# Kernel tuning notes

Hardware: AMD Instinct MI355X
Metric: run time of the kernel (lower is better)

The kernel has to match this reference:

```python
import jax, jax.numpy as jnp
import numpy as np

N = 100_000      # num_nodes
E = 1_600_000    # num_edges (avg degree 16)
D = 64           # embedding_dim
L = 3            # num_layers


def setup_inputs() -> dict:
    key = jax.random.key(0)
    k1, k2 = jax.random.split(key)
    edge_index = jax.random.randint(k1, (2, E), 0, N, dtype=jnp.int64)
    edge_weight = jnp.ones((E,), jnp.float32)
    # nn.init.normal_(std=0.1)
    embedding = 0.1 * jax.random.normal(k2, (N, D), dtype=jnp.float32)
    return {"embedding": embedding, "edge_weight": edge_weight, "edge_index": edge_index}


def reference(embedding, edge_weight, edge_index):
    n = embedding.shape[0]
    self_idx = jnp.arange(n, dtype=edge_index.dtype)
    # add_self_loops: append (i, i) with weight 1 (PyG default fill_value)
    row = jnp.concatenate([edge_index[0], self_idx])  # source j
    col = jnp.concatenate([edge_index[1], self_idx])  # target i
    ew = jnp.concatenate([edge_weight, jnp.ones((n,), embedding.dtype)])
    # degree() counts occurrences of row (unweighted)
    deg = jax.ops.segment_sum(jnp.ones_like(ew), row, num_segments=n)
    deg_inv_sqrt = jnp.where(deg > 0, jax.lax.rsqrt(deg), 0.0)
    norm = deg_inv_sqrt[row] * ew * deg_inv_sqrt[col]  # [E+N]

    x = embedding
    acc = embedding  # running sum of layer-0..L embeddings
    for _ in range(L):
        # gather from source, scale, scatter-add to target (dropout off in eval)
        msg = norm[:, None] * x[row]                       # [E+N, D]
        x = jax.ops.segment_sum(msg, col, num_segments=n)  # [N, D]
        acc = acc + x
    return acc / (L + 1)
```

## Files before the change

### kernel.cpp

```cpp
#include <hip/hip_runtime.h>
#include <stdint.h>

#define DIM 64
#define GB 256
#define GSH 8
#define CH 2048
#define TB1 256
#define HW 25000
#define NSL 256
#define TBH 1024

__device__ __forceinline__ unsigned bf16rne(float f) {
    unsigned u = __float_as_uint(f);
    return (u + 0x7FFFu + ((u >> 16) & 1u)) >> 16;
}
__device__ __forceinline__ unsigned pack2(float lo, float hi) {
    return bf16rne(lo) | (bf16rne(hi) << 16);
}
#define UNPK(u, lo, hi) { lo = __uint_as_float((u) << 16); hi = __uint_as_float((u) & 0xFFFF0000u); }

__global__ void __launch_bounds__(TBH)
hist_kernel(const int* __restrict__ src, const int* __restrict__ dst,
            unsigned* __restrict__ partials, int* __restrict__ bslice,
            int E, int N, int Es, int NB) {
    __shared__ unsigned h8[HW];
    __shared__ int hb[512];
    const int s = blockIdx.x;
    const int nw = (N + 3) >> 2;
    for (int j = threadIdx.x; j < nw; j += TBH) h8[j] = 0;
    for (int j = threadIdx.x; j < 512; j += TBH) hb[j] = 0;
    __syncthreads();
    const int e0 = s * Es, e1 = min(e0 + Es, E);
#pragma unroll 4
    for (int i = e0 + threadIdx.x; i < e1; i += TBH) {
        unsigned sj = (unsigned)src[i];
        unsigned tj = (unsigned)dst[i];
        atomicAdd(&h8[sj >> 2], 1u << ((sj & 3) * 8));
        atomicAdd(&hb[tj >> GSH], 1);
    }
    __syncthreads();
    unsigned* part = partials + (size_t)s * nw;
    for (int j = threadIdx.x; j < nw; j += TBH) part[j] = h8[j];
    for (int j = threadIdx.x; j < NB; j += TBH) bslice[s * 512 + j] = hb[j];
}

__global__ void __launch_bounds__(512)
merge_scan_kernel(const unsigned* __restrict__ partials, const int* __restrict__ bslice,
                  float* __restrict__ dis, int* __restrict__ bucket_base,
                  int* __restrict__ cursor, int* __restrict__ offsets,
                  int nw, int nmerge, int N, int NB) {
    __shared__ int buf[512];
    if ((int)blockIdx.x < nmerge) {
        const int w = blockIdx.x * 512 + threadIdx.x;
        if (w >= nw) return;
        int s0 = 0, s1 = 0, s2 = 0, s3 = 0;
#pragma unroll 8
        for (int s = 0; s < NSL; ++s) {
            unsigned v = partials[(size_t)s * nw + w];
            s0 += v & 255u; s1 += (v >> 8) & 255u;
            s2 += (v >> 16) & 255u; s3 += v >> 24;
        }
        const int nidx = w * 4;
        if (nidx + 3 < N) {
            *(float4*)(dis + nidx) = make_float4(
                rsqrtf((float)s0 + 1.f), rsqrtf((float)s1 + 1.f),
                rsqrtf((float)s2 + 1.f), rsqrtf((float)s3 + 1.f));
        } else {
            if (nidx + 0 < N) dis[nidx + 0] = rsqrtf((float)s0 + 1.f);
            if (nidx + 1 < N) dis[nidx + 1] = rsqrtf((float)s1 + 1.f);
            if (nidx + 2 < N) dis[nidx + 2] = rsqrtf((float)s2 + 1.f);
            if (nidx + 3 < N) dis[nidx + 3] = rsqrtf((float)s3 + 1.f);
        }
    } else {
        const int t = threadIdx.x;
        int v = 0;
        if (t < NB)
            for (int s = 0; s < NSL; ++s) v += bslice[s * 512 + t];
        buf[t] = v;
        __syncthreads();
        for (int off = 1; off < 512; off <<= 1) {
            int add = (t >= off) ? buf[t - off] : 0;
            __syncthreads();
            buf[t] += add;
            __syncthreads();
        }
        if (t < NB) { bucket_base[t] = buf[t] - v; cursor[t] = buf[t] - v; }
        if (t == NB - 1) { bucket_base[NB] = buf[t]; offsets[N] = buf[t]; }
    }
}

__global__ void __launch_bounds__(TB1)
part_conv_kernel(const int* __restrict__ src, const int* __restrict__ dst,
                 const float* __restrict__ ew,
                 int* __restrict__ cursor, int2* __restrict__ staged,
                 const float4* __restrict__ emb4, uint4* __restrict__ x0c,
                 int E, int NB, int npart, int n8) {
    __shared__ int h[512];
    if ((int)blockIdx.x >= npart) {
        const int i = (blockIdx.x - npart) * TB1 + threadIdx.x;
        if (i >= n8) return;
        float4 a = emb4[2 * i], b = emb4[2 * i + 1];
        uint4 o;
        o.x = pack2(a.x, a.y); o.y = pack2(a.z, a.w);
        o.z = pack2(b.x, b.y); o.w = pack2(b.z, b.w);
        x0c[i] = o;
        return;
    }
    const int tid = threadIdx.x;
    const int e0 = blockIdx.x * CH;
    const int e1 = min(e0 + CH, E);
    for (int j = tid; j < 512; j += TB1) h[j] = 0;
    __syncthreads();
    int4 d[CH / (TB1 * 4)];
    int ngrp = 0;
    for (int i = e0 + tid * 4, k = 0; i < e1; i += TB1 * 4, ++k) {
        int4 t;
        if (i + 3 < e1) t = *(const int4*)(dst + i);
        else {
            t.x = dst[i];
            t.y = (i + 1 < e1) ? dst[i + 1] : -1;
            t.z = (i + 2 < e1) ? dst[i + 2] : -1;
            t.w = (i + 3 < e1) ? dst[i + 3] : -1;
        }
        d[k] = t;
        if (t.x >= 0) atomicAdd(&h[t.x >> GSH], 1);
        if (t.y >= 0) atomicAdd(&h[t.y >> GSH], 1);
        if (t.z >= 0) atomicAdd(&h[t.z >> GSH], 1);
        if (t.w >= 0) atomicAdd(&h[t.w >> GSH], 1);
        ngrp = k + 1;
    }
    __syncthreads();
    for (int j = tid; j < NB; j += TB1) {
        int c = h[j];
        h[j] = c ? atomicAdd(&cursor[j], c) : 0;
    }
    __syncthreads();
    for (int i = e0 + tid * 4, k = 0; k < ngrp; i += TB1 * 4, ++k) {
        int4 t = d[k];
        int4 ss = make_int4(0, 0, 0, 0);
        float4 ww = make_float4(0.f, 0.f, 0.f, 0.f);
        if (i + 3 < e1) { ss = *(const int4*)(src + i); ww = *(const float4*)(ew + i); }
        else {
            ss.x = src[i]; ww.x = ew[i];
            if (i + 1 < e1) { ss.y = src[i + 1]; ww.y = ew[i + 1]; }
            if (i + 2 < e1) { ss.z = src[i + 2]; ww.z = ew[i + 2]; }
            if (i + 3 < e1) { ss.w = src[i + 3]; ww.w = ew[i + 3]; }
        }
#define PART1(T, S, W) if ((T) >= 0) { \
        int pos_ = atomicAdd(&h[(T) >> GSH], 1); \
        staged[pos_] = make_int2((S) | (((T) & (GB - 1)) << 20), __float_as_int(W)); }
        PART1(t.x, ss.x, ww.x)
        PART1(t.y, ss.y, ww.y)
        PART1(t.z, ss.z, ww.z)
        PART1(t.w, ss.w, ww.w)
#undef PART1
    }
}

__global__ void __launch_bounds__(256)
place_kernel(const int2* __restrict__ staged, const int* __restrict__ bucket_base,
             const float* __restrict__ dis,
             int* __restrict__ offsets, int2* __restrict__ csr, int N) {
    __shared__ int cnt[GB];
    __shared__ int cur[GB];
    __shared__ int pre[GB + 1];
    __shared__ float disb[GB];
    const int b = blockIdx.x;
    const int n0 = b << GSH;
    const int nb = min(GB, N - n0);
    const int r0 = bucket_base[b], r1 = bucket_base[b + 1];
    cnt[threadIdx.x] = 0;
    disb[threadIdx.x] = (threadIdx.x < nb) ? dis[n0 + threadIdx.x] : 0.f;
    __syncthreads();
    for (int i = r0 + threadIdx.x; i < r1; i += 256)
        atomicAdd(&cnt[(staged[i].x >> 20) & (GB - 1)], 1);
    __syncthreads();
    if (threadIdx.x == 0) {
        int run = r0;
        for (int j = 0; j < nb; ++j) { pre[j] = run; run += cnt[j]; }
        pre[nb] = run;
    }
    __syncthreads();
    if (threadIdx.x < nb) { offsets[n0 + threadIdx.x] = pre[threadIdx.x]; cur[threadIdx.x] = pre[threadIdx.x]; }
    __syncthreads();
    for (int i = r0 + threadIdx.x; i < r1; i += 256) {
        int2 rec = staged[i];
        int tl = (rec.x >> 20) & (GB - 1);
        int s = rec.x & 0xFFFFF;
        int rank = atomicAdd(&cur[tl], 1);
        float w = dis[s] * __int_as_float(rec.y) * disb[tl];
        csr[rank] = make_int2(s, __float_as_int(w));
    }
}

__global__ void __launch_bounds__(256)
prop_kernel(const uint4* __restrict__ xg, const float4* __restrict__ selfF,
            uint4* __restrict__ xstore,
            const int* __restrict__ offsets, const int2* __restrict__ csr,
            const float* __restrict__ dis, int n,
            const float4* __restrict__ embF, const uint4* __restrict__ xaF,
            float4* __restrict__ outF) {
    const int lane = threadIdx.x & 63;
    const int fl  = lane & 7;
    const int sub = lane >> 3;
    const int wave = blockIdx.x * (blockDim.x >> 6) + (threadIdx.x >> 6);
    const int node = wave * 8 + sub;
    if (node >= n) return;

    const int beg = offsets[node];
    const int end = offsets[node + 1];
    const float d = dis[node];
    const float dd = d * d;

    float a0, a1, a2, a3, a4, a5, a6, a7;
    uint4 qs = make_uint4(0, 0, 0, 0);
    if (selfF) {
        float4 s0 = selfF[(size_t)node * 16 + fl * 2];
        float4 s1 = selfF[(size_t)node * 16 + fl * 2 + 1];
        a0 = dd * s0.x; a1 = dd * s0.y; a2 = dd * s0.z; a3 = dd * s0.w;
        a4 = dd * s1.x; a5 = dd * s1.y; a6 = dd * s1.z; a7 = dd * s1.w;
    } else {
        qs = xg[(size_t)node * 8 + fl];
        float l, h;
        UNPK(qs.x, l, h) a0 = dd * l; a1 = dd * h;
        UNPK(qs.y, l, h) a2 = dd * l; a3 = dd * h;
        UNPK(qs.z, l, h) a4 = dd * l; a5 = dd * h;
        UNPK(qs.w, l, h) a6 = dd * l; a7 = dd * h;
    }

#define EDGE(E, Q) { float w_ = __int_as_float((E).y); float l, h; \
    UNPK((Q).x, l, h) a0 = fmaf(w_, l, a0); a1 = fmaf(w_, h, a1); \
    UNPK((Q).y, l, h) a2 = fmaf(w_, l, a2); a3 = fmaf(w_, h, a3); \
    UNPK((Q).z, l, h) a4 = fmaf(w_, l, a4); a5 = fmaf(w_, h, a5); \
    UNPK((Q).w, l, h) a6 = fmaf(w_, l, a6); a7 = fmaf(w_, h, a7); }

    int p = beg;
    for (; p + 8 <= end; p += 8) {
        int2 e0 = csr[p + 0], e1 = csr[p + 1], e2 = csr[p + 2], e3 = csr[p + 3];
        int2 e4 = csr[p + 4], e5 = csr[p + 5], e6 = csr[p + 6], e7 = csr[p + 7];
        uint4 q0 = xg[(size_t)e0.x * 8 + fl];
        uint4 q1 = xg[(size_t)e1.x * 8 + fl];
        uint4 q2 = xg[(size_t)e2.x * 8 + fl];
        uint4 q3 = xg[(size_t)e3.x * 8 + fl];
        uint4 q4 = xg[(size_t)e4.x * 8 + fl];
        uint4 q5 = xg[(size_t)e5.x * 8 + fl];
        uint4 q6 = xg[(size_t)e6.x * 8 + fl];
        uint4 q7 = xg[(size_t)e7.x * 8 + fl];
        EDGE(e0, q0) EDGE(e1, q1) EDGE(e2, q2) EDGE(e3, q3)
        EDGE(e4, q4) EDGE(e5, q5) EDGE(e6, q6) EDGE(e7, q7)
    }
    for (; p + 4 <= end; p += 4) {
        int2 e0 = csr[p + 0], e1 = csr[p + 1], e2 = csr[p + 2], e3 = csr[p + 3];
        uint4 q0 = xg[(size_t)e0.x * 8 + fl];
        uint4 q1 = xg[(size_t)e1.x * 8 + fl];
        uint4 q2 = xg[(size_t)e2.x * 8 + fl];
        uint4 q3 = xg[(size_t)e3.x * 8 + fl];
        EDGE(e0, q0) EDGE(e1, q1) EDGE(e2, q2) EDGE(e3, q3)
    }
    for (; p < end; ++p) {
        int2 e = csr[p];
        uint4 q = xg[(size_t)e.x * 8 + fl];
        EDGE(e, q)
    }
#undef EDGE

    if (outF) {
        float4 eA = embF[(size_t)node * 16 + fl * 2];
        float4 eB = embF[(size_t)node * 16 + fl * 2 + 1];
        uint4 qa = xaF[(size_t)node * 8 + fl];
        float r0 = eA.x + a0, r1 = eA.y + a1, r2 = eA.z + a2, r3 = eA.w + a3;
        float r4 = eB.x + a4, r5 = eB.y + a5, r6 = eB.z + a6, r7 = eB.w + a7;
        float l, h;
        UNPK(qa.x, l, h) r0 += l; r1 += h;
        UNPK(qa.y, l, h) r2 += l; r3 += h;
        UNPK(qa.z, l, h) r4 += l; r5 += h;
        UNPK(qa.w, l, h) r6 += l; r7 += h;
        UNPK(qs.x, l, h) r0 += l; r1 += h;
        UNPK(qs.y, l, h) r2 += l; r3 += h;
        UNPK(qs.z, l, h) r4 += l; r5 += h;
        UNPK(qs.w, l, h) r6 += l; r7 += h;
        outF[(size_t)node * 16 + fl * 2] =
            make_float4(0.25f * r0, 0.25f * r1, 0.25f * r2, 0.25f * r3);
        outF[(size_t)node * 16 + fl * 2 + 1] =
            make_float4(0.25f * r4, 0.25f * r5, 0.25f * r6, 0.25f * r7);
    } else {
        uint4 o;
        o.x = pack2(a0, a1); o.y = pack2(a2, a3);
        o.z = pack2(a4, a5); o.w = pack2(a6, a7);
        xstore[(size_t)node * 8 + fl] = o;
    }
}


extern "C" void kernel_launch(void* const* d_in, const int* in_sizes, int n_in,
                              void* d_out, int out_size, void* d_ws, size_t ws_size,
                              hipStream_t stream) {
    const float* emb = (const float*)d_in[0];
    const float* ew  = (const float*)d_in[1];
    const int*   ei  = (const int*)d_in[2];
    const int E = in_sizes[2] / 2;
    const int N = in_sizes[0] / DIM;
    const int* src = ei;
    const int* dst = ei + E;
    float* out = (float*)d_out;

    const int NB = (N + GB - 1) >> GSH;
    const int Es = (E + NSL - 1) / NSL;
    const int nw = (N + 3) >> 2;

    char* w = (char*)d_ws;
    size_t xSz = ((size_t)N * DIM * 2 + 255) & ~(size_t)255;
    size_t sSz = ((size_t)E * 8 + 255) & ~(size_t)255;
    size_t pSz = ((size_t)NSL * nw * 4 + 255) & ~(size_t)255;
    size_t uSz = xSz > sSz ? xSz : sSz; if (pSz > uSz) uSz = pSz;
    unsigned* partials = (unsigned*)w;
    int2* staged = (int2*)w;
    uint4* xb    = (uint4*)w; w += uSz;
    int2* csr    = (int2*)w; w += sSz;
    uint4* x0c   = (uint4*)w; w += xSz;
    uint4* xa    = (uint4*)w; w += xSz;
    int* offsets = (int*)w; w += ((size_t)(N + 1) * 4 + 255) & ~(size_t)255;
    float* dis   = (float*)w; w += ((size_t)N * 4 + 255) & ~(size_t)255;
    int* bslice      = (int*)w; w += (size_t)NSL * 512 * 4;
    int* bucket_base = (int*)w; w += 513 * 4;
    int* cursor      = (int*)w; w += 512 * 4;

    const int TB = 256;

    hist_kernel<<<NSL, TBH, 0, stream>>>(src, dst, partials, bslice, E, N, Es, NB);

    const int nmerge = (nw + 511) / 512;
    merge_scan_kernel<<<nmerge + 1, 512, 0, stream>>>(partials, bslice, dis,
                                                      bucket_base, cursor, offsets,
                                                      nw, nmerge, N, NB);

    const int n8 = N * DIM / 8;
    const int npart = (E + CH - 1) / CH;
    const int nconv = (n8 + TB - 1) / TB;
    part_conv_kernel<<<npart + nconv, TB1, 0, stream>>>(src, dst, ew, cursor, staged,
                                                        (const float4*)emb, x0c,
                                                        E, NB, npart, n8);
    place_kernel<<<NB, TB, 0, stream>>>(staged, bucket_base, dis, offsets, csr, N);

    dim3 grid((N + 31) / 32), block(TB);
    prop_kernel<<<grid, block, 0, stream>>>(x0c, (const float4*)emb, xa,
                                            offsets, csr, dis, N,
                                            nullptr, nullptr, nullptr);
    prop_kernel<<<grid, block, 0, stream>>>(xa, nullptr, xb,
                                            offsets, csr, dis, N,
                                            nullptr, nullptr, nullptr);
    prop_kernel<<<grid, block, 0, stream>>>(xb, nullptr, nullptr,
                                            offsets, csr, dis, N,
                                            (const float4*)emb, xa, (float4*)out);
}
```

Measured before the change: 274.9 us.

## Gather int8-quantized neighbor features with per-node scales in layers two and three

```diff
diff --git a/kernel.cpp b/kernel.cpp
--- a/kernel.cpp
+++ b/kernel.cpp
@@ -4,7 +4,7 @@
 #define DIM 64
 #define GB 256
 #define GSH 8
-#define CH 2048
+#define CH 4096
 #define TB1 256
 #define HW 25000
 #define NSL 256
@@ -193,13 +193,16 @@
     }
 }
 
+template<int MODE>
 __global__ void __launch_bounds__(256)
-prop_kernel(const uint4* __restrict__ xg, const float4* __restrict__ selfF,
-            uint4* __restrict__ xstore,
-            const int* __restrict__ offsets, const int2* __restrict__ csr,
-            const float* __restrict__ dis, int n,
-            const float4* __restrict__ embF, const uint4* __restrict__ xaF,
-            float4* __restrict__ outF) {
+prop_t(const uint4* __restrict__ xgB, const uint2* __restrict__ xg8,
+       const float* __restrict__ scIn,
+       const float4* __restrict__ selfF, const uint4* __restrict__ selfB,
+       uint4* __restrict__ st16, uint2* __restrict__ st8, float* __restrict__ scOut,
+       const int* __restrict__ offsets, const int2* __restrict__ csr,
+       const float* __restrict__ dis, int n,
+       const float4* __restrict__ embF, const uint4* __restrict__ xaF,
+       float4* __restrict__ outF) {
     const int lane = threadIdx.x & 63;
     const int fl  = lane & 7;
     const int sub = lane >> 3;
@@ -214,13 +217,13 @@
 
     float a0, a1, a2, a3, a4, a5, a6, a7;
     uint4 qs = make_uint4(0, 0, 0, 0);
-    if (selfF) {
+    if (MODE == 0) {
         float4 s0 = selfF[(size_t)node * 16 + fl * 2];
         float4 s1 = selfF[(size_t)node * 16 + fl * 2 + 1];
         a0 = dd * s0.x; a1 = dd * s0.y; a2 = dd * s0.z; a3 = dd * s0.w;
         a4 = dd * s1.x; a5 = dd * s1.y; a6 = dd * s1.z; a7 = dd * s1.w;
     } else {
-        qs = xg[(size_t)node * 8 + fl];
+        qs = selfB[(size_t)node * 8 + fl];
         float l, h;
         UNPK(qs.x, l, h) a0 = dd * l; a1 = dd * h;
         UNPK(qs.y, l, h) a2 = dd * l; a3 = dd * h;
@@ -228,43 +231,70 @@
         UNPK(qs.w, l, h) a6 = dd * l; a7 = dd * h;
     }
 
-#define EDGE(E, Q) { float w_ = __int_as_float((E).y); float l, h; \
+#define EDGEB(E, Q) { float w_ = __int_as_float((E).y); float l, h; \
     UNPK((Q).x, l, h) a0 = fmaf(w_, l, a0); a1 = fmaf(w_, h, a1); \
     UNPK((Q).y, l, h) a2 = fmaf(w_, l, a2); a3 = fmaf(w_, h, a3); \
     UNPK((Q).z, l, h) a4 = fmaf(w_, l, a4); a5 = fmaf(w_, h, a5); \
     UNPK((Q).w, l, h) a6 = fmaf(w_, l, a6); a7 = fmaf(w_, h, a7); }
+#define EDGE8(E, G, SC) { float w_ = __int_as_float((E).y) * (SC); \
+    a0 = fmaf(w_, (float)(int)(signed char)((G).x      ), a0); \
+    a1 = fmaf(w_, (float)(int)(signed char)((G).x >>  8), a1); \
+    a2 = fmaf(w_, (float)(int)(signed char)((G).x >> 16), a2); \
+    a3 = fmaf(w_, (float)(int)(signed char)((G).x >> 24), a3); \
+    a4 = fmaf(w_, (float)(int)(signed char)((G).y      ), a4); \
+    a5 = fmaf(w_, (float)(int)(signed char)((G).y >>  8), a5); \
+    a6 = fmaf(w_, (float)(int)(signed char)((G).y >> 16), a6); \
+    a7 = fmaf(w_, (float)(int)(signed char)((G).y >> 24), a7); }
 
     int p = beg;
-    for (; p + 8 <= end; p += 8) {
-        int2 e0 = csr[p + 0], e1 = csr[p + 1], e2 = csr[p + 2], e3 = csr[p + 3];
-        int2 e4 = csr[p + 4], e5 = csr[p + 5], e6 = csr[p + 6], e7 = csr[p + 7];
-        uint4 q0 = xg[(size_t)e0.x * 8 + fl];
-        uint4 q1 = xg[(size_t)e1.x * 8 + fl];
-        uint4 q2 = xg[(size_t)e2.x * 8 + fl];
-        uint4 q3 = xg[(size_t)e3.x * 8 + fl];
-        uint4 q4 = xg[(size_t)e4.x * 8 + fl];
-        uint4 q5 = xg[(size_t)e5.x * 8 + fl];
-        uint4 q6 = xg[(size_t)e6.x * 8 + fl];
-        uint4 q7 = xg[(size_t)e7.x * 8 + fl];
-        EDGE(e0, q0) EDGE(e1, q1) EDGE(e2, q2) EDGE(e3, q3)
-        EDGE(e4, q4) EDGE(e5, q5) EDGE(e6, q6) EDGE(e7, q7)
-    }
-    for (; p + 4 <= end; p += 4) {
-        int2 e0 = csr[p + 0], e1 = csr[p + 1], e2 = csr[p + 2], e3 = csr[p + 3];
-        uint4 q0 = xg[(size_t)e0.x * 8 + fl];
-        uint4 q1 = xg[(size_t)e1.x * 8 + fl];
-        uint4 q2 = xg[(size_t)e2.x * 8 + fl];
-        uint4 q3 = xg[(size_t)e3.x * 8 + fl];
-        EDGE(e0, q0) EDGE(e1, q1) EDGE(e2, q2) EDGE(e3, q3)
-    }
-    for (; p < end; ++p) {
-        int2 e = csr[p];
-        uint4 q = xg[(size_t)e.x * 8 + fl];
-        EDGE(e, q)
-    }
-#undef EDGE
-
-    if (outF) {
+    if (MODE == 0) {
+        for (; p + 8 <= end; p += 8) {
+            int2 e0 = csr[p + 0], e1 = csr[p + 1], e2 = csr[p + 2], e3 = csr[p + 3];
+            int2 e4 = csr[p + 4], e5 = csr[p + 5], e6 = csr[p + 6], e7 = csr[p + 7];
+            uint4 q0 = xgB[(size_t)e0.x * 8 + fl];
+            uint4 q1 = xgB[(size_t)e1.x * 8 + fl];
+            uint4 q2 = xgB[(size_t)e2.x * 8 + fl];
+            uint4 q3 = xgB[(size_t)e3.x * 8 + fl];
+            uint4 q4 = xgB[(size_t)e4.x * 8 + fl];
+            uint4 q5 = xgB[(size_t)e5.x * 8 + fl];
+            uint4 q6 = xgB[(size_t)e6.x * 8 + fl];
+            uint4 q7 = xgB[(size_t)e7.x * 8 + fl];
+            EDGEB(e0, q0) EDGEB(e1, q1) EDGEB(e2, q2) EDGEB(e3, q3)
+            EDGEB(e4, q4) EDGEB(e5, q5) EDGEB(e6, q6) EDGEB(e7, q7)
+        }
+        for (; p < end; ++p) {
+            int2 e = csr[p];
+            uint4 q = xgB[(size_t)e.x * 8 + fl];
+            EDGEB(e, q)
+        }
+    } else {
+        for (; p + 8 <= end; p += 8) {
+            int2 e0 = csr[p + 0], e1 = csr[p + 1], e2 = csr[p + 2], e3 = csr[p + 3];
+            int2 e4 = csr[p + 4], e5 = csr[p + 5], e6 = csr[p + 6], e7 = csr[p + 7];
+            float c0 = scIn[e0.x], c1 = scIn[e1.x], c2 = scIn[e2.x], c3 = scIn[e3.x];
+            float c4 = scIn[e4.x], c5 = scIn[e5.x], c6 = scIn[e6.x], c7 = scIn[e7.x];
+            uint2 g0 = xg8[(size_t)e0.x * 8 + fl];
+            uint2 g1 = xg8[(size_t)e1.x * 8 + fl];
+            uint2 g2 = xg8[(size_t)e2.x * 8 + fl];
+            uint2 g3 = xg8[(size_t)e3.x * 8 + fl];
+            uint2 g4 = xg8[(size_t)e4.x * 8 + fl];
+            uint2 g5 = xg8[(size_t)e5.x * 8 + fl];
+            uint2 g6 = xg8[(size_t)e6.x * 8 + fl];
+            uint2 g7 = xg8[(size_t)e7.x * 8 + fl];
+            EDGE8(e0, g0, c0) EDGE8(e1, g1, c1) EDGE8(e2, g2, c2) EDGE8(e3, g3, c3)
+            EDGE8(e4, g4, c4) EDGE8(e5, g5, c5) EDGE8(e6, g6, c6) EDGE8(e7, g7, c7)
+        }
+        for (; p < end; ++p) {
+            int2 e = csr[p];
+            float c = scIn[e.x];
+            uint2 g = xg8[(size_t)e.x * 8 + fl];
+            EDGE8(e, g, c)
+        }
+    }
+#undef EDGEB
+#undef EDGE8
+
+    if (MODE == 2) {
         float4 eA = embF[(size_t)node * 16 + fl * 2];
         float4 eB = embF[(size_t)node * 16 + fl * 2 + 1];
         uint4 qa = xaF[(size_t)node * 8 + fl];
@@ -287,7 +317,25 @@
         uint4 o;
         o.x = pack2(a0, a1); o.y = pack2(a2, a3);
         o.z = pack2(a4, a5); o.w = pack2(a6, a7);
-        xstore[(size_t)node * 8 + fl] = o;
+        st16[(size_t)node * 8 + fl] = o;
+        float m = fmaxf(fabsf(a0), fabsf(a1));
+        m = fmaxf(m, fmaxf(fabsf(a2), fabsf(a3)));
+        m = fmaxf(m, fmaxf(fabsf(a4), fabsf(a5)));
+        m = fmaxf(m, fmaxf(fabsf(a6), fabsf(a7)));
+        m = fmaxf(m, __shfl_xor(m, 1));
+        m = fmaxf(m, __shfl_xor(m, 2));
+        m = fmaxf(m, __shfl_xor(m, 4));
+        m = fmaxf(m, 1e-20f);
+        const float inv = 127.0f / m;
+        int i0 = (int)rintf(a0 * inv), i1 = (int)rintf(a1 * inv);
+        int i2 = (int)rintf(a2 * inv), i3 = (int)rintf(a3 * inv);
+        int i4 = (int)rintf(a4 * inv), i5 = (int)rintf(a5 * inv);
+        int i6 = (int)rintf(a6 * inv), i7 = (int)rintf(a7 * inv);
+        uint2 o8;
+        o8.x = (i0 & 255) | ((i1 & 255) << 8) | ((i2 & 255) << 16) | ((unsigned)(i3 & 255) << 24);
+        o8.y = (i4 & 255) | ((i5 & 255) << 8) | ((i6 & 255) << 16) | ((unsigned)(i7 & 255) << 24);
+        st8[(size_t)node * 8 + fl] = o8;
+        if (fl == 0) scOut[node] = m * (1.0f / 127.0f);
     }
 }
 
@@ -310,17 +358,22 @@
 
     char* w = (char*)d_ws;
     size_t xSz = ((size_t)N * DIM * 2 + 255) & ~(size_t)255;
+    size_t qSz = ((size_t)N * DIM + 255) & ~(size_t)255;
     size_t sSz = ((size_t)E * 8 + 255) & ~(size_t)255;
     size_t pSz = ((size_t)NSL * nw * 4 + 255) & ~(size_t)255;
     size_t uSz = xSz > sSz ? xSz : sSz; if (pSz > uSz) uSz = pSz;
     unsigned* partials = (unsigned*)w;
     int2* staged = (int2*)w;
-    uint4* xb    = (uint4*)w; w += uSz;
+    uint4* xb16  = (uint4*)w; w += uSz;
     int2* csr    = (int2*)w; w += sSz;
     uint4* x0c   = (uint4*)w; w += xSz;
-    uint4* xa    = (uint4*)w; w += xSz;
+    uint4* xa16  = (uint4*)w; w += xSz;
+    uint2* xa8   = (uint2*)w; w += qSz;
+    uint2* xb8   = (uint2*)w; w += qSz;
     int* offsets = (int*)w; w += ((size_t)(N + 1) * 4 + 255) & ~(size_t)255;
     float* dis   = (float*)w; w += ((size_t)N * 4 + 255) & ~(size_t)255;
+    float* sa    = (float*)w; w += ((size_t)N * 4 + 255) & ~(size_t)255;
+    float* sb    = (float*)w; w += ((size_t)N * 4 + 255) & ~(size_t)255;
     int* bslice      = (int*)w; w += (size_t)NSL * 512 * 4;
     int* bucket_base = (int*)w; w += 513 * 4;
     int* cursor      = (int*)w; w += 512 * 4;
@@ -343,13 +396,19 @@
     place_kernel<<<NB, TB, 0, stream>>>(staged, bucket_base, dis, offsets, csr, N);
 
     dim3 grid((N + 31) / 32), block(TB);
-    prop_kernel<<<grid, block, 0, stream>>>(x0c, (const float4*)emb, xa,
-                                            offsets, csr, dis, N,
-                                            nullptr, nullptr, nullptr);
-    prop_kernel<<<grid, block, 0, stream>>>(xa, nullptr, xb,
-                                            offsets, csr, dis, N,
-                                            nullptr, nullptr, nullptr);
-    prop_kernel<<<grid, block, 0, stream>>>(xb, nullptr, nullptr,
-                                            offsets, csr, dis, N,
-                                            (const float4*)emb, xa, (float4*)out);
-}
+    prop_t<0><<<grid, block, 0, stream>>>(x0c, nullptr, nullptr,
+                                          (const float4*)emb, nullptr,
+                                          xa16, xa8, sa,
+                                          offsets, csr, dis, N,
+                                          nullptr, nullptr, nullptr);
+    prop_t<1><<<grid, block, 0, stream>>>(nullptr, xa8, sa,
+                                          nullptr, xa16,
+                                          xb16, xb8, sb,
+                                          offsets, csr, dis, N,
+                                          nullptr, nullptr, nullptr);
+    prop_t<2><<<grid, block, 0, stream>>>(nullptr, xb8, sb,
+                                          nullptr, xb16,
+                                          nullptr, nullptr, nullptr,
+                                          offsets, csr, dis, N,
+                                          (const float4*)emb, xa16, (float4*)out);
+}
```

Measured after the change: 269.2 us. 1.02x faster.
